# Optimization experiments

Measured on AMD Instinct MI355X. Metric: run time of the kernel, lower is better.

The kernel has to match this reference:

```python
import jax, jax.numpy as jnp
from jax import lax
import numpy as np

GRID_SIZE = 3
SPLINE_ORDER = 2
N_BASIS = GRID_SIZE + SPLINE_ORDER  # 5
_H = 2.0 / GRID_SIZE  # grid_range [-1, 1]
# extended uniform grid, shape (1, grid_size + 2*spline_order + 1) = (1, 8)
GRID = (jnp.arange(-SPLINE_ORDER, GRID_SIZE + SPLINE_ORDER + 1, dtype=jnp.float32) * _H - 1.0)[None, :]


def b_splines(x):
    """Cox-de Boor B-spline bases. x: (..., F) -> (..., F, N_BASIS)."""
    x = x[..., None]
    g = GRID
    bases = ((x >= g[:, :-1]) & (x < g[:, 1:])).astype(x.dtype)
    for p in range(1, SPLINE_ORDER + 1):
        left = (x - g[:, :-(p + 1)]) / (g[:, p:-1] - g[:, :-(p + 1)])
        right = (g[:, p + 1:] - x) / (g[:, p + 1:] - g[:, 1:-p])
        bases = left * bases[..., :-1] + right * bases[..., 1:]
    return bases


def kan_conv(x, base_w, spline_w, scaler):
    """Unfold-based KAN conv: x NCHW -> NCHW. base_w (O,F), spline_w (O,F,K), scaler (O,F)."""
    # patches: (B, C*kh*kw, H', W'), channel-major feature ordering like torch unfold
    p = lax.conv_general_dilated_patches(x, (4, 4), (2, 2), ((1, 1), (1, 1)))
    f = jnp.transpose(p, (0, 2, 3, 1))  # (B, H', W', F)
    base = jax.nn.relu(f) @ base_w.T
    spl = jnp.einsum('bhwfk,ofk->bhwo', b_splines(f), spline_w * scaler[..., None])
    return jnp.transpose(base + spl, (0, 3, 1, 2))


def batchnorm(x, gamma, beta):
    # train-mode BN over (B,H,W) per channel, eps=1e-5 (torch default)
    m = x.mean((0, 2, 3), keepdims=True)
    v = x.var((0, 2, 3), keepdims=True)
    return (x - m) * lax.rsqrt(v + 1e-5) * gamma[None, :, None, None] + beta[None, :, None, None]


def setup_inputs() -> dict:
    key = jax.random.key(0)
    ks = jax.random.split(key, 32)
    B = 512
    chans = [(3, 32), (32, 64), (64, 128), (128, 128)]
    inp = {"x": jax.random.normal(ks[0], (B, 3, 32, 32), jnp.float32)}
    i = 1
    for li, (cin, cout) in enumerate(chans, start=1):
        F = cin * 16
        inp[f"bw{li}"] = jax.random.normal(ks[i], (cout, F), jnp.float32) * (0.8 / np.sqrt(F)); i += 1
        inp[f"sw{li}"] = jax.random.normal(ks[i], (cout, F, N_BASIS), jnp.float32) * (0.8 / np.sqrt(F)); i += 1
        inp[f"sc{li}"] = jnp.ones((cout, F), jnp.float32) + 0.05 * jax.random.normal(ks[i], (cout, F), jnp.float32); i += 1
    for bi, c in [(1, 64), (2, 128), (3, 128)]:
        inp[f"g{bi}"] = jnp.ones((c,), jnp.float32)
        inp[f"b{bi}"] = jnp.zeros((c,), jnp.float32)
    inp["fc_w"] = jax.random.normal(ks[i], (1, 128), jnp.float32) * (1.0 / np.sqrt(128)); i += 1
    inp["fc_b"] = jnp.zeros((1,), jnp.float32)
    return inp


def reference(x, bw1, sw1, sc1, bw2, sw2, sc2, bw3, sw3, sc3, bw4, sw4, sc4,
              g1, b1, g2, b2, g3, b3, fc_w, fc_b):
    h = kan_conv(x, bw1, sw1, sc1)                     # (B,32,16,16)
    h = kan_conv(h, bw2, sw2, sc2)                     # (B,64,8,8)
    h = batchnorm(h, g1, b1)
    h = kan_conv(h, bw3, sw3, sc3)                     # (B,128,4,4)
    h = batchnorm(h, g2, b2)
    h = kan_conv(h, bw4, sw4, sc4)                     # (B,128,2,2)
    h = batchnorm(h, g3, b3)
    h = h.mean((2, 3))                                 # AdaptiveAvgPool2d(1) + Flatten -> (B,128)
    return jax.nn.sigmoid(h @ fc_w.T + fc_b)           # (B,1)
```

## Files before the change

kernel.cpp:

```cpp
#include <hip/hip_runtime.h>
#include <hip/hip_bf16.h>
#include <math.h>

#define DEVINL __device__ __forceinline__

typedef short short8 __attribute__((ext_vector_type(8)));
typedef float f32x4 __attribute__((ext_vector_type(4)));

DEVINL unsigned short f2bf(float f) {
    union { float f; unsigned int u; } c; c.f = f;
    unsigned int u = c.u;
    return (unsigned short)((u + 0x7fffu + ((u >> 16) & 1u)) >> 16);
}

DEVINL unsigned int packbf2(float a, float b) {
    union { __hip_bfloat162 h; unsigned int u; } c;
    c.h = __float22bfloat162_rn(make_float2(a, b));
    return c.u;
}

DEVINL void gload_lds16(const unsigned int* g, unsigned int* l) {
    __builtin_amdgcn_global_load_lds((const __attribute__((address_space(1))) unsigned int*)g,
                                     (__attribute__((address_space(3))) unsigned int*)l, 16, 0, 0);
}

DEVINL uint4 expand_frag(float v) {
    float relu = fmaxf(v, 0.f);
    float u = fmaf(v, 1.5f, 3.5f);
    float fj = floorf(u);
    int j = (int)fj;
    float t = u - fj;
    float omt = 1.f - t;
    float v2 = 0.5f * omt * omt;
    float v1 = fmaf(t, omt, 0.5f);
    float v0 = 0.5f * t * t;
    float b[5];
#pragma unroll
    for (int i = 0; i < 5; ++i)
        b[i] = (i == j) ? v0 : (i == j - 1) ? v1 : (i == j - 2) ? v2 : 0.f;
    uint4 r;
    r.x = packbf2(relu, b[0]);
    r.y = packbf2(b[1], b[2]);
    r.z = packbf2(b[3], b[4]);
    r.w = 0u;
    return r;
}

DEVINL void prep_one(int idx, int F, int NTT, const float* __restrict__ bw,
                     const float* __restrict__ sw, const float* __restrict__ sc,
                     unsigned short* __restrict__ wf) {
    int j = idx & 7;
    int lane = (idx >> 3) & 63;
    int t = idx >> 9;
    int ks = t & 3;
    int t2 = t >> 2;
    int nt = t2 % NTT;
    int c = t2 / NTT;
    int k = ks * 32 + ((lane >> 4) << 3) + j;
    int tap = k >> 3, s = k & 7;
    int f = c * 16 + tap;
    int o = nt * 16 + (lane & 15);
    float v = 0.f;
    if (s == 0) v = bw[o * F + f];
    else if (s <= 5) v = sw[(o * F + f) * 5 + (s - 1)] * sc[o * F + f];
    wf[idx] = f2bf(v);
}

__global__ __launch_bounds__(256) void prep_all(
    const float* __restrict__ bw1, const float* __restrict__ sw1, const float* __restrict__ sc1,
    const float* __restrict__ bw2, const float* __restrict__ sw2, const float* __restrict__ sc2,
    const float* __restrict__ bw3, const float* __restrict__ sw3, const float* __restrict__ sc3,
    const float* __restrict__ bw4, const float* __restrict__ sw4, const float* __restrict__ sc4,
    unsigned short* __restrict__ wf1, unsigned short* __restrict__ wf2,
    unsigned short* __restrict__ wf3, unsigned short* __restrict__ wf4) {
    int idx = blockIdx.x * 256 + threadIdx.x;
    const int N1 = 3 * 32 * 128;
    const int N2 = 32 * 64 * 128;
    const int N3 = 64 * 128 * 128;
    const int N4 = 128 * 128 * 128;
    if (idx < N1) prep_one(idx, 48, 2, bw1, sw1, sc1, wf1);
    else if (idx < N1 + N2) prep_one(idx - N1, 512, 4, bw2, sw2, sc2, wf2);
    else if (idx < N1 + N2 + N3) prep_one(idx - N1 - N2, 1024, 8, bw3, sw3, sc3, wf3);
    else if (idx < N1 + N2 + N3 + N4) prep_one(idx - N1 - N2 - N3, 2048, 8, bw4, sw4, sc4, wf4);
}

template <int CIN, int COUTT, int NSP, int HOUT, int WOUT, int WM, int WN, int MT,
          int CPS, int UB, bool HASBN, int BNS, int NBN, bool SPLITOUT, int RPAD>
__global__ __launch_bounds__(256) void kan_conv_fused(
    const float* __restrict__ in, const unsigned short* __restrict__ wf,
    const float* __restrict__ part, const float* __restrict__ gamma,
    const float* __restrict__ beta, float* __restrict__ out) {
    constexpr int HIN = HOUT * 2, WIN = WOUT * 2, W2 = WOUT;
    constexpr int COUT = COUTT / NSP;
    constexpr int NTT = COUTT / 16;
    constexpr int NT = COUT / 16;
    constexpr int NTW = NT / WN;
    constexpr int BM = WM * MT * 16;
    constexpr int IMG_POS = HOUT * WOUT;
    constexpr int NIMG = BM / IMG_POS;
    constexpr int RS = WIN + RPAD;
    constexpr int IMG_STRIDE = HIN * RS + 1;
    constexpr int ASLOTS = NIMG * IMG_STRIDE + 1;
    constexpr int M_TOT = 512 * IMG_POS;
    constexpr int EV = NIMG * HIN * WIN;
    constexpr int EITER = (EV + 255) / 256;
    static_assert(WM * WN == 4, "4 waves");
    static_assert(CPS % UB == 0, "UB divides CPS");

    __shared__ uint4 A_e[UB][ASLOTS];
    __shared__ uint4 B_l[UB][COUT * 16];

    const int tid = threadIdx.x;
    const int lane = tid & 63;
    const int w = tid >> 6;
    const int wm = w % WM;
    const int wn = w / WM;
    const int g = lane >> 4;
    const int r16 = lane & 15;
    const int m0 = blockIdx.x * BM;
    const int b0 = m0 / IMG_POS;
    const int nh = (NSP > 1) ? ((int)blockIdx.y % NSP) : 0;
    const int kslice = (NSP > 1) ? ((int)blockIdx.y / NSP) : (SPLITOUT ? (int)blockIdx.y : 0);
    const int c0 = SPLITOUT ? kslice * CPS : 0;

    int aoff[MT];
    int vmask = 0;
#pragma unroll
    for (int mt = 0; mt < MT; ++mt) {
        int p = (wm * MT + mt) * 16 + r16;
        int m = m0 + p;
        int ow = m % WOUT;
        int oh = (m / WOUT) % HOUT;
        int bl = p / IMG_POS;
        int iw = 2 * ow - 1 + g;
        bool iv = (iw >= 0) && (iw < WIN);
        aoff[mt] = 1 + bl * IMG_STRIDE + (2 * oh) * RS + (iw & 1) * W2 + (iw >> 1);
#pragma unroll
        for (int ks = 0; ks < 4; ++ks) {
            bool vv = iv && !(oh == 0 && ks == 0) && !(oh == HOUT - 1 && ks == 3);
            vmask |= (vv ? 1 : 0) << (mt * 4 + ks);
        }
    }

    if (tid < UB) A_e[tid][0] = expand_frag(0.f);

    f32x4 acc[MT][NTW];
#pragma unroll
    for (int mt = 0; mt < MT; ++mt)
#pragma unroll
        for (int n = 0; n < NTW; ++n) acc[mt][n] = f32x4{0.f, 0.f, 0.f, 0.f};

    for (int cc = 0; cc < CPS; cc += UB) {
#pragma unroll
        for (int u = 0; u < UB; ++u) {
            const int ch = c0 + cc + u;
            const unsigned int* bsrc = (const unsigned int*)wf + ((size_t)ch * NTT + nh * NT) * 1024;
            unsigned int* bdst = (unsigned int*)&B_l[u][0];
#pragma unroll
            for (int r2 = 0; r2 < NT; ++r2)
                gload_lds16(bsrc + (r2 << 10) + tid * 4, bdst + (r2 << 10) + tid * 4);
        }
#pragma unroll
        for (int u = 0; u < UB; ++u) {
            const int ch = c0 + cc + u;
            float bsc = 1.f, bsh = 0.f;
            if (HASBN) {
                float sm = 0.f, s2 = 0.f;
#pragma unroll 4
                for (int s = 0; s < BNS; ++s) {
                    sm += part[(ch * BNS + s) * 2];
                    s2 += part[(ch * BNS + s) * 2 + 1];
                }
                const float invN = 1.f / (float)NBN;
                float mean = sm * invN;
                float var = s2 * invN - mean * mean;
                float rs = rsqrtf(var + 1e-5f);
                bsc = gamma[ch] * rs;
                bsh = beta[ch] - mean * bsc;
            }
#pragma unroll
            for (int ii = 0; ii < EITER; ++ii) {
                int e = tid + ii * 256;
                if ((EV % 256 == 0) || e < EV) {
                    int bl = e / (HIN * WIN);
                    int r = e - bl * (HIN * WIN);
                    int ih = r / WIN;
                    int iw = r - ih * WIN;
                    float v = in[(((size_t)(b0 + bl) * CIN + ch) * HIN + ih) * WIN + iw];
                    if (HASBN) v = fmaf(v, bsc, bsh);
                    A_e[u][1 + bl * IMG_STRIDE + ih * RS + (iw & 1) * W2 + (iw >> 1)] = expand_frag(v);
                }
            }
        }
        __syncthreads();
#pragma unroll
        for (int u = 0; u < UB; ++u) {
#pragma unroll
            for (int ks = 0; ks < 4; ++ks) {
                short8 bf[NTW];
#pragma unroll
                for (int n = 0; n < NTW; ++n)
                    bf[n] = *(const short8*)&B_l[u][(((wn * NTW + n) * 4 + ks) << 6) + lane];
#pragma unroll
                for (int mt = 0; mt < MT; ++mt) {
                    int slot = ((vmask >> (mt * 4 + ks)) & 1) ? (aoff[mt] + (ks - 1) * RS) : 0;
                    short8 af = *(const short8*)&A_e[u][slot];
#pragma unroll
                    for (int n = 0; n < NTW; ++n)
                        acc[mt][n] = __builtin_amdgcn_mfma_f32_16x16x32_bf16(af, bf[n], acc[mt][n], 0, 0, 0);
                }
            }
        }
        __syncthreads();
    }

    const int colo = lane & 15;
    const int row4 = (lane >> 4) * 4;
#pragma unroll
    for (int mt = 0; mt < MT; ++mt) {
#pragma unroll
        for (int n = 0; n < NTW; ++n) {
            int o = nh * COUT + (wn * NTW + n) * 16 + colo;
#pragma unroll
            for (int rr = 0; rr < 4; ++rr) {
                int p = (wm * MT + mt) * 16 + row4 + rr;
                int m = m0 + p;
                if (SPLITOUT) {
                    out[((size_t)kslice * M_TOT + m) * COUTT + o] = acc[mt][n][rr];
                } else {
                    int ow = m % WOUT;
                    int t = m / WOUT;
                    int oh = t % HOUT;
                    int b = t / HOUT;
                    out[((b * COUTT + o) * HOUT + oh) * WOUT + ow] = acc[mt][n][rr];
                }
            }
        }
    }
}

template <int NS, int COUT, int HOUT, int WOUT>
__global__ __launch_bounds__(256) void reduce_split(const float* __restrict__ P,
                                                    float* __restrict__ out) {
    constexpr int M = 512 * HOUT * WOUT;
    int idx4 = blockIdx.x * 256 + threadIdx.x;
    if (idx4 >= M * COUT / 4) return;
    f32x4 s = {0.f, 0.f, 0.f, 0.f};
#pragma unroll
    for (int i = 0; i < NS; ++i) {
        f32x4 v = *(const f32x4*)&P[(size_t)i * M * COUT + idx4 * 4];
        s += v;
    }
    int o0 = (idx4 * 4) % COUT;
    int m = (idx4 * 4) / COUT;
    int ow = m % WOUT;
    int t = m / WOUT;
    int oh = t % HOUT;
    int b = t / HOUT;
#pragma unroll
    for (int q = 0; q < 4; ++q)
        out[((b * COUT + o0 + q) * HOUT + oh) * WOUT + ow] = s[q];
}

template <int C, int HW, int S>
__global__ __launch_bounds__(256) void bn_partial(const float* __restrict__ a,
                                                  float* __restrict__ part) {
    constexpr int BS = 512 / S;
    constexpr int NE = BS * HW;
    int c = blockIdx.x / S, s = blockIdx.x % S;
    int tid = threadIdx.x;
    float sm = 0.f, s2 = 0.f;
    for (int e = tid; e < NE; e += 256) {
        int b = s * BS + e / HW;
        int hw = e % HW;
        float v = a[((size_t)b * C + c) * HW + hw];
        sm += v;
        s2 += v * v;
    }
    __shared__ float r0[256], r1[256];
    r0[tid] = sm; r1[tid] = s2;
    __syncthreads();
    for (int off = 128; off > 0; off >>= 1) {
        if (tid < off) { r0[tid] += r0[tid + off]; r1[tid] += r1[tid + off]; }
        __syncthreads();
    }
    if (tid == 0) {
        part[(c * S + s) * 2] = r0[0];
        part[(c * S + s) * 2 + 1] = r1[0];
    }
}

__global__ void head_ker(const float* __restrict__ a4, const float* __restrict__ part3,
                         const float* __restrict__ g3, const float* __restrict__ b3,
                         const float* __restrict__ fcw, const float* __restrict__ fcb,
                         float* __restrict__ out) {
    int b = blockIdx.x;
    int lane = threadIdx.x;
    float acc = 0.0f;
#pragma unroll
    for (int j = 0; j < 2; ++j) {
        int o = lane + 64 * j;
        float sm = 0.f, s2 = 0.f;
#pragma unroll
        for (int s = 0; s < 8; ++s) {
            sm += part3[(o * 8 + s) * 2];
            s2 += part3[(o * 8 + s) * 2 + 1];
        }
        float mean = sm * (1.f / 2048.f);
        float var = s2 * (1.f / 2048.f) - mean * mean;
        float rs = rsqrtf(var + 1e-5f);
        float scl = g3[o] * rs;
        float sh = b3[o] - mean * scl;
        const float* p = a4 + (b * 128 + o) * 4;
        float sv = p[0] + p[1] + p[2] + p[3];
        float pooled = fmaf(sv * 0.25f, scl, sh);
        acc = fmaf(pooled, fcw[o], acc);
    }
#pragma unroll
    for (int off = 32; off > 0; off >>= 1) acc += __shfl_down(acc, off);
    if (lane == 0) out[b] = 1.0f / (1.0f + expf(-(acc + fcb[0])));
}

extern "C" void kernel_launch(void* const* d_in, const int* in_sizes, int n_in,
                              void* d_out, int out_size, void* d_ws, size_t ws_size,
                              hipStream_t stream) {
    const float* x   = (const float*)d_in[0];
    const float* bw1 = (const float*)d_in[1];
    const float* sw1 = (const float*)d_in[2];
    const float* sc1 = (const float*)d_in[3];
    const float* bw2 = (const float*)d_in[4];
    const float* sw2 = (const float*)d_in[5];
    const float* sc2 = (const float*)d_in[6];
    const float* bw3 = (const float*)d_in[7];
    const float* sw3 = (const float*)d_in[8];
    const float* sc3 = (const float*)d_in[9];
    const float* bw4 = (const float*)d_in[10];
    const float* sw4 = (const float*)d_in[11];
    const float* sc4 = (const float*)d_in[12];
    const float* g1  = (const float*)d_in[13];
    const float* b1  = (const float*)d_in[14];
    const float* g2  = (const float*)d_in[15];
    const float* b2  = (const float*)d_in[16];
    const float* g3  = (const float*)d_in[17];
    const float* b3  = (const float*)d_in[18];
    const float* fcw = (const float*)d_in[19];
    const float* fcb = (const float*)d_in[20];

    float* ws = (float*)d_ws;
    float* a1 = ws;
    float* a2 = a1 + 4194304;
    float* a3 = a2 + 2097152;
    float* a4 = a3 + 1048576;
    unsigned short* wf1 = (unsigned short*)(a4 + 262144);
    unsigned short* wf2 = wf1 + 12288;
    unsigned short* wf3 = wf2 + 262144;
    unsigned short* wf4 = wf3 + 1048576;
    float* part1 = (float*)(wf4 + 2097152);
    float* part2 = part1 + 2048;
    float* part3 = part2 + 4096;
    float* P3 = a1;
    float* P4 = a2;

    prep_all<<<13360, 256, 0, stream>>>(bw1, sw1, sc1, bw2, sw2, sc2,
                                        bw3, sw3, sc3, bw4, sw4, sc4,
                                        wf1, wf2, wf3, wf4);

    kan_conv_fused<3, 32, 1, 16, 16, 4, 1, 4, 3, 3, false, 1, 1, false, 0>
        <<<512, 256, 0, stream>>>(x, wf1, nullptr, nullptr, nullptr, a1);
    kan_conv_fused<32, 64, 2, 8, 8, 4, 1, 2, 32, 4, false, 1, 1, false, 0>
        <<<dim3(256, 2), 256, 0, stream>>>(a1, wf2, nullptr, nullptr, nullptr, a2);
    bn_partial<64, 64, 16><<<1024, 256, 0, stream>>>(a2, part1);
    kan_conv_fused<64, 128, 2, 4, 4, 4, 1, 2, 16, 2, true, 16, 32768, true, 1>
        <<<dim3(64, 8), 256, 0, stream>>>(a2, wf3, part1, g1, b1, P3);
    reduce_split<4, 128, 4, 4><<<1024, 256, 0, stream>>>(P3, a3);
    bn_partial<128, 16, 16><<<2048, 256, 0, stream>>>(a3, part2);
    kan_conv_fused<128, 128, 2, 2, 2, 4, 1, 1, 16, 2, true, 16, 8192, true, 0>
        <<<dim3(32, 16), 256, 0, stream>>>(a3, wf4, part2, g2, b2, P4);
    reduce_split<8, 128, 2, 2><<<256, 256, 0, stream>>>(P4, a4);
    bn_partial<128, 4, 8><<<1024, 256, 0, stream>>>(a4, part3);
    head_ker<<<512, 64, 0, stream>>>(a4, part3, g3, b3, fcw, fcb, (float*)d_out);
}
```

Baseline: 144.7 us.

## Load B fragments directly from global memory and vectorize weight prep

The conv kernel no longer stages weight fragments into LDS with global_load_lds. Each wave now reads its short8 B fragments straight from global memory (likely L2-resident) inside the MFMA loop, which frees LDS and may raise occupancy. The prep kernel now handles one whole 8-element fragment per thread and writes it as a uint4, cutting the thread count eightfold and repeated index math. The cost is global-memory latency exposed directly in the inner loop, and redundant loads across waves and blocks.

```diff
diff --git a/kernel.cpp b/kernel.cpp
--- a/kernel.cpp
+++ b/kernel.cpp
@@ -17,11 +17,6 @@
     union { __hip_bfloat162 h; unsigned int u; } c;
     c.h = __float22bfloat162_rn(make_float2(a, b));
     return c.u;
-}
-
-DEVINL void gload_lds16(const unsigned int* g, unsigned int* l) {
-    __builtin_amdgcn_global_load_lds((const __attribute__((address_space(1))) unsigned int*)g,
-                                     (__attribute__((address_space(3))) unsigned int*)l, 16, 0, 0);
 }
 
 DEVINL uint4 expand_frag(float v) {
@@ -46,24 +41,31 @@
     return r;
 }
 
-DEVINL void prep_one(int idx, int F, int NTT, const float* __restrict__ bw,
-                     const float* __restrict__ sw, const float* __restrict__ sc,
-                     unsigned short* __restrict__ wf) {
-    int j = idx & 7;
-    int lane = (idx >> 3) & 63;
-    int t = idx >> 9;
+DEVINL void prep_frag(int fi, int F, int NTT, const float* __restrict__ bw,
+                      const float* __restrict__ sw, const float* __restrict__ sc,
+                      unsigned short* __restrict__ wf) {
+    int lane = fi & 63;
+    int t = fi >> 6;
     int ks = t & 3;
     int t2 = t >> 2;
     int nt = t2 % NTT;
     int c = t2 / NTT;
-    int k = ks * 32 + ((lane >> 4) << 3) + j;
-    int tap = k >> 3, s = k & 7;
+    int tap = ks * 4 + (lane >> 4);
     int f = c * 16 + tap;
     int o = nt * 16 + (lane & 15);
-    float v = 0.f;
-    if (s == 0) v = bw[o * F + f];
-    else if (s <= 5) v = sw[(o * F + f) * 5 + (s - 1)] * sc[o * F + f];
-    wf[idx] = f2bf(v);
+    float scv = sc[o * F + f];
+    float b = bw[o * F + f];
+    float s0 = sw[(o * F + f) * 5 + 0] * scv;
+    float s1 = sw[(o * F + f) * 5 + 1] * scv;
+    float s2 = sw[(o * F + f) * 5 + 2] * scv;
+    float s3 = sw[(o * F + f) * 5 + 3] * scv;
+    float s4 = sw[(o * F + f) * 5 + 4] * scv;
+    uint4 r;
+    r.x = packbf2(b, s0);
+    r.y = packbf2(s1, s2);
+    r.z = packbf2(s3, s4);
+    r.w = 0u;
+    *(uint4*)&wf[(size_t)fi * 8] = r;
 }
 
 __global__ __launch_bounds__(256) void prep_all(
@@ -73,15 +75,15 @@
     const float* __restrict__ bw4, const float* __restrict__ sw4, const float* __restrict__ sc4,
     unsigned short* __restrict__ wf1, unsigned short* __restrict__ wf2,
     unsigned short* __restrict__ wf3, unsigned short* __restrict__ wf4) {
-    int idx = blockIdx.x * 256 + threadIdx.x;
-    const int N1 = 3 * 32 * 128;
-    const int N2 = 32 * 64 * 128;
-    const int N3 = 64 * 128 * 128;
-    const int N4 = 128 * 128 * 128;
-    if (idx < N1) prep_one(idx, 48, 2, bw1, sw1, sc1, wf1);
-    else if (idx < N1 + N2) prep_one(idx - N1, 512, 4, bw2, sw2, sc2, wf2);
-    else if (idx < N1 + N2 + N3) prep_one(idx - N1 - N2, 1024, 8, bw3, sw3, sc3, wf3);
-    else if (idx < N1 + N2 + N3 + N4) prep_one(idx - N1 - N2 - N3, 2048, 8, bw4, sw4, sc4, wf4);
+    int fi = blockIdx.x * 256 + threadIdx.x;
+    const int N1 = 3 * 32 * 16;
+    const int N2 = 32 * 64 * 16;
+    const int N3 = 64 * 128 * 16;
+    const int N4 = 128 * 128 * 16;
+    if (fi < N1) prep_frag(fi, 48, 2, bw1, sw1, sc1, wf1);
+    else if (fi < N1 + N2) prep_frag(fi - N1, 512, 4, bw2, sw2, sc2, wf2);
+    else if (fi < N1 + N2 + N3) prep_frag(fi - N1 - N2, 1024, 8, bw3, sw3, sc3, wf3);
+    else if (fi < N1 + N2 + N3 + N4) prep_frag(fi - N1 - N2 - N3, 2048, 8, bw4, sw4, sc4, wf4);
 }
 
 template <int CIN, int COUTT, int NSP, int HOUT, int WOUT, int WM, int WN, int MT,
@@ -108,7 +110,6 @@
     static_assert(CPS % UB == 0, "UB divides CPS");
 
     __shared__ uint4 A_e[UB][ASLOTS];
-    __shared__ uint4 B_l[UB][COUT * 16];
 
     const int tid = threadIdx.x;
     const int lane = tid & 63;
@@ -151,15 +152,6 @@
         for (int n = 0; n < NTW; ++n) acc[mt][n] = f32x4{0.f, 0.f, 0.f, 0.f};
 
     for (int cc = 0; cc < CPS; cc += UB) {
-#pragma unroll
-        for (int u = 0; u < UB; ++u) {
-            const int ch = c0 + cc + u;
-            const unsigned int* bsrc = (const unsigned int*)wf + ((size_t)ch * NTT + nh * NT) * 1024;
-            unsigned int* bdst = (unsigned int*)&B_l[u][0];
-#pragma unroll
-            for (int r2 = 0; r2 < NT; ++r2)
-                gload_lds16(bsrc + (r2 << 10) + tid * 4, bdst + (r2 << 10) + tid * 4);
-        }
 #pragma unroll
         for (int u = 0; u < UB; ++u) {
             const int ch = c0 + cc + u;
@@ -195,12 +187,14 @@
         __syncthreads();
 #pragma unroll
         for (int u = 0; u < UB; ++u) {
+            const int ch = c0 + cc + u;
+            const unsigned short* wfc = wf + (((size_t)ch * NTT + nh * NT) << 11);
 #pragma unroll
             for (int ks = 0; ks < 4; ++ks) {
                 short8 bf[NTW];
 #pragma unroll
                 for (int n = 0; n < NTW; ++n)
-                    bf[n] = *(const short8*)&B_l[u][(((wn * NTW + n) * 4 + ks) << 6) + lane];
+                    bf[n] = *(const short8*)&wfc[((((wn * NTW + n) << 2) + ks) << 9) + (lane << 3)];
 #pragma unroll
                 for (int mt = 0; mt < MT; ++mt) {
                     int slot = ((vmask >> (mt * 4 + ks)) & 1) ? (aoff[mt] + (ks - 1) * RS) : 0;
@@ -361,9 +355,9 @@
     float* P3 = a1;
     float* P4 = a2;
 
-    prep_all<<<13360, 256, 0, stream>>>(bw1, sw1, sc1, bw2, sw2, sc2,
-                                        bw3, sw3, sc3, bw4, sw4, sc4,
-                                        wf1, wf2, wf3, wf4);
+    prep_all<<<1670, 256, 0, stream>>>(bw1, sw1, sc1, bw2, sw2, sc2,
+                                       bw3, sw3, sc3, bw4, sw4, sc4,
+                                       wf1, wf2, wf3, wf4);
 
     kan_conv_fused<3, 32, 1, 16, 16, 4, 1, 4, 3, 3, false, 1, 1, false, 0>
         <<<512, 256, 0, stream>>>(x, wf1, nullptr, nullptr, nullptr, a1);
```

Result: slower. 205.0 us (+41.7%).
